# Kernel optimization log

Hardware: AMD Instinct MI355X
Metric: run time of the kernel (lower is better)

The kernel has to match this reference:

```python
import jax, jax.numpy as jnp
import numpy as np

N = 50000      # nodes
E = 800000     # edges (avg degree 16)
H = 2          # heads
IN = 128       # in_channels
OUT = 32       # out_channels


def setup_inputs() -> dict:
    key = jax.random.key(0)
    k1, k2, k3, k4, k5, k6 = jax.random.split(key, 6)
    x = jax.random.normal(k1, (N, IN), jnp.float32)
    pos = jax.random.normal(k2, (N, 3), jnp.float32)
    # xavier-ish scaled params
    W = jax.random.normal(k3, (H, IN, OUT), jnp.float32) * (1.0 / np.sqrt(IN))
    attn = jax.random.normal(k4, (H, 2 * OUT), jnp.float32) * (1.0 / np.sqrt(2 * OUT))
    row = jax.random.randint(k5, (E,), 0, N, dtype=jnp.int32)
    col = jax.random.randint(k6, (E,), 0, N, dtype=jnp.int32)
    return {"x": x, "pos": pos, "W": W, "attn": attn, "row": row, "col": col}


def _segment_softmax(logits, seg, n):
    # numerically-stable softmax grouped by destination node `seg`
    m = jax.ops.segment_max(logits, seg, num_segments=n)
    m = jnp.where(jnp.isfinite(m), m, 0.0)          # empty segments -> 0
    z = jnp.exp(logits - m[seg])
    s = jax.ops.segment_sum(z, seg, num_segments=n)
    return z / jnp.maximum(s[seg], 1e-16)


def reference(x, pos, W, attn, row, col):
    n = x.shape[0]
    out = jnp.einsum('ni,hio->hno', x, W)           # [H,N,h] per-head projection
    # add self loops (num_nodes), PyG fills self-loop edge weight with 1
    loop = jnp.arange(n, dtype=row.dtype)
    row2 = jnp.concatenate([row, loop])             # [E'] = E + N
    col2 = jnp.concatenate([col, loop])
    d = jnp.sqrt(jnp.sum((pos[col] - pos[row]) ** 2, axis=-1))   # [E]
    dist = jnp.maximum(jnp.concatenate([d, jnp.ones(n, x.dtype)]), 1e-6)  # [E']
    src = out[:, row2]                              # edge gather  [H,E',h]
    e = jnp.concatenate([src, src], axis=-1)        # duplicated src (per source) [H,E',2h]
    logits = jnp.einsum('hed,hd->he', e, attn)      # per-edge attention score [H,E']
    alpha = jax.vmap(lambda l: _segment_softmax(l, row2, n))(logits)  # [H,E']
    s = e.sum(axis=-1) * alpha / dist               # weighted per-edge scalar [H,E']
    node = jax.vmap(lambda v: jax.ops.segment_sum(v, row2, num_segments=n))(s)  # [H,N]
    return node[:, row2] - node[:, col2]            # indexed subtraction [H,E']
```

## Files before the change

kernel.cpp:

```cpp
#include <hip/hip_runtime.h>

#define IN_DIM 128
#define OUT_DIM 32
#define NHEAD 2
#define BINSZ 12500
#define NSTRIPE 64
#define THREADS 1024
#define PBLOCKS 256
#define FIX 32.0f
#define INV_FALLBACK 128.0f
#define LDS_CNT_SHIFT 25
#define U16_INV_MASK 0x1FFFu
#define U16_CNT_SHIFT 13
#define FB_NODES 32
#define FB_GROUPS 8

__global__ __launch_bounds__(THREADS) void k_main(
        const int* __restrict__ row, const int* __restrict__ col,
        const float* __restrict__ pos, const float* __restrict__ x,
        const float* __restrict__ W,
        unsigned short* __restrict__ partial, float* __restrict__ Dbig,
        float2* __restrict__ S2, int N, int E, int nbins, int eblocks) {
    __shared__ __align__(16) unsigned acc[BINSZ];
    const int b = blockIdx.x;
    if (b < eblocks) {
        const int bin  = b % nbins;
        const int s    = b / nbins;
        const int base = bin * BINSZ;
        const int lim  = min(BINSZ, N - base);
        for (int j = threadIdx.x; j < BINSZ; j += THREADS) acc[j] = 0u;
        __syncthreads();

        const int slen = (E + NSTRIPE - 1) / NSTRIPE;
        const int e0 = s * slen;
        const int e1 = min(e0 + slen, E);

        auto accum = [&](int r, int c) {
            int rb = r - base;
            if ((unsigned)rb < (unsigned)lim) {
                float dx = pos[c * 3 + 0] - pos[r * 3 + 0];
                float dy = pos[c * 3 + 1] - pos[r * 3 + 1];
                float dz = pos[c * 3 + 2] - pos[r * 3 + 2];
                float inv = 1.0f / fmaxf(sqrtf(dx * dx + dy * dy + dz * dz), 1e-6f);
                if (inv <= INV_FALLBACK) {
                    atomicAdd(&acc[rb], (1u << LDS_CNT_SHIFT) + (unsigned)(inv * FIX + 0.5f));
                } else {
                    atomicAdd(&acc[rb], 1u << LDS_CNT_SHIFT);
                    atomicAdd(&Dbig[r], inv);
                }
            }
        };

        if (((e0 | e1) & 3) == 0) {
            for (int e = e0 + (int)threadIdx.x * 4; e < e1; e += THREADS * 4) {
                int4 r4 = *(const int4*)(row + e);
                int4 c4 = *(const int4*)(col + e);
                accum(r4.x, c4.x); accum(r4.y, c4.y);
                accum(r4.z, c4.z); accum(r4.w, c4.w);
            }
        } else {
            for (int e = e0 + (int)threadIdx.x; e < e1; e += THREADS)
                accum(row[e], col[e]);
        }

        __syncthreads();
        unsigned short* dst = partial + (size_t)s * N + base;
        for (int j = threadIdx.x; j < lim; j += THREADS) {
            unsigned v   = acc[j];
            unsigned cnt = v >> LDS_CNT_SHIFT;
            unsigned inv = v & ((1u << LDS_CNT_SHIFT) - 1u);
            cnt = min(cnt, 7u);
            inv = min(inv, U16_INV_MASK);
            dst[j] = (unsigned short)((cnt << U16_CNT_SHIFT) | inv);
        }
    } else {
        float* wl = (float*)acc;
        if (threadIdx.x < NHEAD * IN_DIM) {
            const float4* wp = (const float4*)(W + threadIdx.x * OUT_DIM);
            float s = 0.f;
            #pragma unroll
            for (int q = 0; q < 8; ++q) {
                float4 v = wp[q];
                s += (v.x + v.y) + (v.z + v.w);
            }
            wl[threadIdx.x] = s;
        }
        __syncthreads();

        const int lid = threadIdx.x & 15;
        const float4* wv = (const float4*)wl;
        float4 w0a = wv[lid * 2],      w0b = wv[lid * 2 + 1];
        float4 w1a = wv[32 + lid * 2], w1b = wv[32 + lid * 2 + 1];

        const int g      = (b - eblocks) * (THREADS / 16) + (threadIdx.x >> 4);
        const int stride = (gridDim.x - eblocks) * (THREADS / 16);
        for (int i = g; i < N; i += stride) {
            const float4* xp = (const float4*)(x + (size_t)i * IN_DIM);
            float4 xa = xp[lid * 2], xb = xp[lid * 2 + 1];
            float s0 = (xa.x * w0a.x + xa.y * w0a.y + xa.z * w0a.z + xa.w * w0a.w)
                     + (xb.x * w0b.x + xb.y * w0b.y + xb.z * w0b.z + xb.w * w0b.w);
            float s1 = (xa.x * w1a.x + xa.y * w1a.y + xa.z * w1a.z + xa.w * w1a.w)
                     + (xb.x * w1b.x + xb.y * w1b.y + xb.z * w1b.z + xb.w * w1b.w);
            #pragma unroll
            for (int off = 8; off >= 1; off >>= 1) {
                s0 += __shfl_xor(s0, off, 16);
                s1 += __shfl_xor(s1, off, 16);
            }
            if (lid == 0) S2[i] = make_float2(s0, s1);
        }
    }
}

__global__ void k_fold(const unsigned short* __restrict__ partial,
                       const float* __restrict__ Dbig,
                       const float2* __restrict__ S2,
                       float2* __restrict__ node2, int N) {
    __shared__ unsigned sh[FB_GROUPS][FB_NODES];
    const int il = threadIdx.x & (FB_NODES - 1);
    const int g  = threadIdx.x >> 5;
    const int i  = blockIdx.x * FB_NODES + il;
    unsigned isum = 0, csum = 0;
    if (i < N) {
        #pragma unroll
        for (int q = 0; q < 8; ++q) {
            unsigned v = partial[(size_t)(g * 8 + q) * N + i];
            isum += v & U16_INV_MASK;
            csum += v >> U16_CNT_SHIFT;
        }
    }
    sh[g][il] = (csum << 20) | isum;
    __syncthreads();
    if (g == 0 && i < N) {
        unsigned tot = 0;
        #pragma unroll
        for (int q = 0; q < FB_GROUPS; ++q) tot += sh[q][il];
        float invsum = (float)(tot & 0xFFFFFu) * (1.0f / FIX) + Dbig[i];
        float fac = 2.0f * (1.0f + invsum) / (1.0f + (float)(tot >> 20));
        float2 sv = S2[i];
        node2[i] = make_float2(sv.x * fac, sv.y * fac);
    }
}

__global__ void k_out2(const int* __restrict__ row, const int* __restrict__ col,
                       const float2* __restrict__ node2,
                       float* __restrict__ out, int E, int M) {
    int k = (blockIdx.x * blockDim.x + threadIdx.x) * 2;
    if (k >= M) return;
    float2 a = make_float2(0.f, 0.f), b = make_float2(0.f, 0.f);
    if (k < E) {
        int2 r2 = *(const int2*)(row + k);
        int2 c2 = *(const int2*)(col + k);
        float2 nr0 = node2[r2.x], nc0 = node2[c2.x];
        float2 nr1 = node2[r2.y], nc1 = node2[c2.y];
        a = make_float2(nr0.x - nc0.x, nr1.x - nc1.x);
        b = make_float2(nr0.y - nc0.y, nr1.y - nc1.y);
    }
    *(float2*)(out + k)     = a;
    *(float2*)(out + M + k) = b;
}

__global__ void k_out1(const int* __restrict__ row, const int* __restrict__ col,
                       const float2* __restrict__ node2,
                       float* __restrict__ out, int E, int M) {
    int k = blockIdx.x * blockDim.x + threadIdx.x;
    if (k >= M) return;
    float o0 = 0.f, o1 = 0.f;
    if (k < E) {
        float2 nr = node2[row[k]], nc = node2[col[k]];
        o0 = nr.x - nc.x;
        o1 = nr.y - nc.y;
    }
    out[k]     = o0;
    out[M + k] = o1;
}

extern "C" void kernel_launch(void* const* d_in, const int* in_sizes, int n_in,
                              void* d_out, int out_size, void* d_ws, size_t ws_size,
                              hipStream_t stream) {
    const float* x   = (const float*)d_in[0];
    const float* pos = (const float*)d_in[1];
    const float* W   = (const float*)d_in[2];
    const int* row = (const int*)d_in[4];
    const int* col = (const int*)d_in[5];
    float* out = (float*)d_out;

    const int N = in_sizes[0] / IN_DIM;
    const int E = in_sizes[4];
    const int M = E + N;
    const int nbins = (N + BINSZ - 1) / BINSZ;
    const int eblocks = nbins * NSTRIPE;

    float2* S2    = (float2*)d_ws;
    float2* node2 = S2 + N;
    float*  Dbig  = (float*)(node2 + N);
    unsigned short* partial = (unsigned short*)(Dbig + N);

    hipMemsetAsync(Dbig, 0, (size_t)N * sizeof(float), stream);

    k_main<<<eblocks + PBLOCKS, THREADS, 0, stream>>>(
        row, col, pos, x, W, partial, Dbig, S2, N, E, nbins, eblocks);
    k_fold<<<(N + FB_NODES - 1) / FB_NODES, FB_NODES * FB_GROUPS, 0, stream>>>(
        partial, Dbig, S2, node2, N);
    if (((E | M) & 1) == 0)
        k_out2<<<((M >> 1) + 255) / 256, 256, 0, stream>>>(row, col, node2, out, E, M);
    else
        k_out1<<<(M + 255) / 256, 256, 0, stream>>>(row, col, node2, out, E, M);
}
```

Before: 40.99 us.

## Fuse edge binning, fold and output into one cooperative kernel with grid syncs

Replaces the memset plus three separate kernel launches with a single cooperative kernel of 256 blocks that runs the edge-binning/projection, fold and edge-output phases separated by grid.sync(). The partial buffer widens to 32-bit words with a different count/fixed-point split, which removes the Dbig atomic fallback for large inverse distances and the memset that cleared it. Stripes are halved, so each edge block scans more edges. Launch and inter-kernel gaps should shrink, at the cost of fewer edge blocks, grid-barrier overhead and possible fixed-point overflow when inverse distances are very large.

```diff
diff --git a/kernel.cpp b/kernel.cpp
--- a/kernel.cpp
+++ b/kernel.cpp
@@ -1,28 +1,26 @@
 #include <hip/hip_runtime.h>
+#include <hip/hip_cooperative_groups.h>
+
+namespace cg = cooperative_groups;
 
 #define IN_DIM 128
 #define OUT_DIM 32
 #define NHEAD 2
 #define BINSZ 12500
-#define NSTRIPE 64
+#define NSTRIPE 32
 #define THREADS 1024
-#define PBLOCKS 256
-#define FIX 32.0f
-#define INV_FALLBACK 128.0f
-#define LDS_CNT_SHIFT 25
-#define U16_INV_MASK 0x1FFFu
-#define U16_CNT_SHIFT 13
-#define FB_NODES 32
-#define FB_GROUPS 8
-
-__global__ __launch_bounds__(THREADS) void k_main(
+#define GRID 256
+#define FIX 16.0f
+#define CSHIFT 26
+#define IMASK ((1u << CSHIFT) - 1u)
+
+__device__ __forceinline__ void phase_edges_proj(
+        unsigned* acc, int b, int nblocks,
         const int* __restrict__ row, const int* __restrict__ col,
         const float* __restrict__ pos, const float* __restrict__ x,
         const float* __restrict__ W,
-        unsigned short* __restrict__ partial, float* __restrict__ Dbig,
-        float2* __restrict__ S2, int N, int E, int nbins, int eblocks) {
-    __shared__ __align__(16) unsigned acc[BINSZ];
-    const int b = blockIdx.x;
+        unsigned* __restrict__ partial, float2* __restrict__ S2,
+        int N, int E, int nbins, int eblocks) {
     if (b < eblocks) {
         const int bin  = b % nbins;
         const int s    = b / nbins;
@@ -42,12 +40,7 @@
                 float dy = pos[c * 3 + 1] - pos[r * 3 + 1];
                 float dz = pos[c * 3 + 2] - pos[r * 3 + 2];
                 float inv = 1.0f / fmaxf(sqrtf(dx * dx + dy * dy + dz * dz), 1e-6f);
-                if (inv <= INV_FALLBACK) {
-                    atomicAdd(&acc[rb], (1u << LDS_CNT_SHIFT) + (unsigned)(inv * FIX + 0.5f));
-                } else {
-                    atomicAdd(&acc[rb], 1u << LDS_CNT_SHIFT);
-                    atomicAdd(&Dbig[r], inv);
-                }
+                atomicAdd(&acc[rb], (1u << CSHIFT) + (unsigned)(inv * FIX + 0.5f));
             }
         };
 
@@ -64,15 +57,8 @@
         }
 
         __syncthreads();
-        unsigned short* dst = partial + (size_t)s * N + base;
-        for (int j = threadIdx.x; j < lim; j += THREADS) {
-            unsigned v   = acc[j];
-            unsigned cnt = v >> LDS_CNT_SHIFT;
-            unsigned inv = v & ((1u << LDS_CNT_SHIFT) - 1u);
-            cnt = min(cnt, 7u);
-            inv = min(inv, U16_INV_MASK);
-            dst[j] = (unsigned short)((cnt << U16_CNT_SHIFT) | inv);
-        }
+        unsigned* dst = partial + (size_t)s * N + base;
+        for (int j = threadIdx.x; j < lim; j += THREADS) dst[j] = acc[j];
     } else {
         float* wl = (float*)acc;
         if (threadIdx.x < NHEAD * IN_DIM) {
@@ -93,7 +79,7 @@
         float4 w1a = wv[32 + lid * 2], w1b = wv[32 + lid * 2 + 1];
 
         const int g      = (b - eblocks) * (THREADS / 16) + (threadIdx.x >> 4);
-        const int stride = (gridDim.x - eblocks) * (THREADS / 16);
+        const int stride = (nblocks - eblocks) * (THREADS / 16);
         for (int i = g; i < N; i += stride) {
             const float4* xp = (const float4*)(x + (size_t)i * IN_DIM);
             float4 xa = xp[lid * 2], xb = xp[lid * 2 + 1];
@@ -111,67 +97,114 @@
     }
 }
 
-__global__ void k_fold(const unsigned short* __restrict__ partial,
-                       const float* __restrict__ Dbig,
-                       const float2* __restrict__ S2,
-                       float2* __restrict__ node2, int N) {
-    __shared__ unsigned sh[FB_GROUPS][FB_NODES];
-    const int il = threadIdx.x & (FB_NODES - 1);
-    const int g  = threadIdx.x >> 5;
-    const int i  = blockIdx.x * FB_NODES + il;
-    unsigned isum = 0, csum = 0;
-    if (i < N) {
-        #pragma unroll
-        for (int q = 0; q < 8; ++q) {
-            unsigned v = partial[(size_t)(g * 8 + q) * N + i];
-            isum += v & U16_INV_MASK;
-            csum += v >> U16_CNT_SHIFT;
-        }
-    }
-    sh[g][il] = (csum << 20) | isum;
-    __syncthreads();
-    if (g == 0 && i < N) {
-        unsigned tot = 0;
-        #pragma unroll
-        for (int q = 0; q < FB_GROUPS; ++q) tot += sh[q][il];
-        float invsum = (float)(tot & 0xFFFFFu) * (1.0f / FIX) + Dbig[i];
-        float fac = 2.0f * (1.0f + invsum) / (1.0f + (float)(tot >> 20));
-        float2 sv = S2[i];
-        node2[i] = make_float2(sv.x * fac, sv.y * fac);
-    }
-}
-
-__global__ void k_out2(const int* __restrict__ row, const int* __restrict__ col,
-                       const float2* __restrict__ node2,
-                       float* __restrict__ out, int E, int M) {
-    int k = (blockIdx.x * blockDim.x + threadIdx.x) * 2;
-    if (k >= M) return;
-    float2 a = make_float2(0.f, 0.f), b = make_float2(0.f, 0.f);
-    if (k < E) {
-        int2 r2 = *(const int2*)(row + k);
-        int2 c2 = *(const int2*)(col + k);
-        float2 nr0 = node2[r2.x], nc0 = node2[c2.x];
-        float2 nr1 = node2[r2.y], nc1 = node2[c2.y];
-        a = make_float2(nr0.x - nc0.x, nr1.x - nc1.x);
-        b = make_float2(nr0.y - nc0.y, nr1.y - nc1.y);
-    }
-    *(float2*)(out + k)     = a;
-    *(float2*)(out + M + k) = b;
-}
-
-__global__ void k_out1(const int* __restrict__ row, const int* __restrict__ col,
-                       const float2* __restrict__ node2,
-                       float* __restrict__ out, int E, int M) {
-    int k = blockIdx.x * blockDim.x + threadIdx.x;
-    if (k >= M) return;
-    float o0 = 0.f, o1 = 0.f;
-    if (k < E) {
-        float2 nr = node2[row[k]], nc = node2[col[k]];
-        o0 = nr.x - nc.x;
-        o1 = nr.y - nc.y;
-    }
-    out[k]     = o0;
-    out[M + k] = o1;
+__device__ __forceinline__ void phase_fold(
+        unsigned* acc, int b, int nblocks,
+        const unsigned* __restrict__ partial, const float2* __restrict__ S2,
+        float2* __restrict__ node2, int N) {
+    unsigned* sh_i = acc;
+    unsigned* sh_c = acc + 1024;
+    const int il = threadIdx.x & 63;
+    const int g  = threadIdx.x >> 6;
+    const int ntiles = (N + 63) / 64;
+    for (int tile = b; tile < ntiles; tile += nblocks) {
+        const int i = tile * 64 + il;
+        unsigned isum = 0, csum = 0;
+        if (i < N) {
+            #pragma unroll
+            for (int q = 0; q < NSTRIPE / 16; ++q) {
+                unsigned v = partial[(size_t)(g * (NSTRIPE / 16) + q) * N + i];
+                isum += v & IMASK;
+                csum += v >> CSHIFT;
+            }
+        }
+        sh_i[g * 64 + il] = isum;
+        sh_c[g * 64 + il] = csum;
+        __syncthreads();
+        if (g == 0 && i < N) {
+            unsigned ti = 0, tc = 0;
+            #pragma unroll
+            for (int q = 0; q < 16; ++q) {
+                ti += sh_i[q * 64 + il];
+                tc += sh_c[q * 64 + il];
+            }
+            float invsum = (float)ti * (1.0f / FIX);
+            float fac = 2.0f * (1.0f + invsum) / (1.0f + (float)tc);
+            float2 sv = S2[i];
+            node2[i] = make_float2(sv.x * fac, sv.y * fac);
+        }
+        __syncthreads();
+    }
+}
+
+__device__ __forceinline__ void phase_out(
+        int b, int nblocks,
+        const int* __restrict__ row, const int* __restrict__ col,
+        const float2* __restrict__ node2, float* __restrict__ out,
+        int E, int M) {
+    const bool mEven = ((M & 1) == 0);
+    const int base   = (b * THREADS + (int)threadIdx.x) * 2;
+    const int stride = nblocks * THREADS * 2;
+    for (int k = base; k < M; k += stride) {
+        float o0a = 0.f, o1a = 0.f, o0b = 0.f, o1b = 0.f;
+        const bool pair = (k + 1 < M);
+        if (k < E) {
+            float2 nr = node2[row[k]], nc = node2[col[k]];
+            o0a = nr.x - nc.x; o1a = nr.y - nc.y;
+        }
+        if (pair && k + 1 < E) {
+            float2 nr = node2[row[k + 1]], nc = node2[col[k + 1]];
+            o0b = nr.x - nc.x; o1b = nr.y - nc.y;
+        }
+        if (pair && mEven) {
+            *(float2*)(out + k)     = make_float2(o0a, o0b);
+            *(float2*)(out + M + k) = make_float2(o1a, o1b);
+        } else {
+            out[k] = o0a;         out[M + k] = o1a;
+            if (pair) { out[k + 1] = o0b; out[M + k + 1] = o1b; }
+        }
+    }
+}
+
+__global__ __launch_bounds__(THREADS, 4) void k_fused(
+        const int* __restrict__ row, const int* __restrict__ col,
+        const float* __restrict__ pos, const float* __restrict__ x,
+        const float* __restrict__ W,
+        unsigned* __restrict__ partial, float2* __restrict__ S2,
+        float2* __restrict__ node2, float* __restrict__ out,
+        int N, int E, int M, int nbins, int eblocks) {
+    __shared__ __align__(16) unsigned acc[BINSZ];
+    cg::grid_group grid = cg::this_grid();
+    phase_edges_proj(acc, blockIdx.x, GRID, row, col, pos, x, W,
+                     partial, S2, N, E, nbins, eblocks);
+    grid.sync();
+    phase_fold(acc, blockIdx.x, GRID, partial, S2, node2, N);
+    grid.sync();
+    phase_out(blockIdx.x, GRID, row, col, node2, out, E, M);
+}
+
+__global__ __launch_bounds__(THREADS) void k_A(
+        const int* __restrict__ row, const int* __restrict__ col,
+        const float* __restrict__ pos, const float* __restrict__ x,
+        const float* __restrict__ W,
+        unsigned* __restrict__ partial, float2* __restrict__ S2,
+        int N, int E, int nbins, int eblocks) {
+    __shared__ __align__(16) unsigned acc[BINSZ];
+    phase_edges_proj(acc, blockIdx.x, gridDim.x, row, col, pos, x, W,
+                     partial, S2, N, E, nbins, eblocks);
+}
+
+__global__ __launch_bounds__(THREADS) void k_B(
+        const unsigned* __restrict__ partial, const float2* __restrict__ S2,
+        float2* __restrict__ node2, int N) {
+    __shared__ __align__(16) unsigned acc[2048];
+    phase_fold(acc, blockIdx.x, gridDim.x, partial, S2, node2, N);
+}
+
+__global__ __launch_bounds__(THREADS) void k_C(
+        const int* __restrict__ row, const int* __restrict__ col,
+        const float2* __restrict__ node2, float* __restrict__ out,
+        int E, int M) {
+    phase_out(blockIdx.x, gridDim.x, row, col, node2, out, E, M);
 }
 
 extern "C" void kernel_launch(void* const* d_in, const int* in_sizes, int n_in,
@@ -184,25 +217,27 @@
     const int* col = (const int*)d_in[5];
     float* out = (float*)d_out;
 
-    const int N = in_sizes[0] / IN_DIM;
-    const int E = in_sizes[4];
-    const int M = E + N;
-    const int nbins = (N + BINSZ - 1) / BINSZ;
-    const int eblocks = nbins * NSTRIPE;
+    int N = in_sizes[0] / IN_DIM;
+    int E = in_sizes[4];
+    int M = E + N;
+    int nbins = (N + BINSZ - 1) / BINSZ;
+    int eblocks = nbins * NSTRIPE;
+    if (eblocks > GRID - 32) eblocks = GRID - 32;
 
     float2* S2    = (float2*)d_ws;
     float2* node2 = S2 + N;
-    float*  Dbig  = (float*)(node2 + N);
-    unsigned short* partial = (unsigned short*)(Dbig + N);
-
-    hipMemsetAsync(Dbig, 0, (size_t)N * sizeof(float), stream);
-
-    k_main<<<eblocks + PBLOCKS, THREADS, 0, stream>>>(
-        row, col, pos, x, W, partial, Dbig, S2, N, E, nbins, eblocks);
-    k_fold<<<(N + FB_NODES - 1) / FB_NODES, FB_NODES * FB_GROUPS, 0, stream>>>(
-        partial, Dbig, S2, node2, N);
-    if (((E | M) & 1) == 0)
-        k_out2<<<((M >> 1) + 255) / 256, 256, 0, stream>>>(row, col, node2, out, E, M);
-    else
-        k_out1<<<(M + 255) / 256, 256, 0, stream>>>(row, col, node2, out, E, M);
-}
+    unsigned* partial = (unsigned*)(node2 + N);
+
+    void* args[] = { (void*)&row, (void*)&col, (void*)&pos, (void*)&x, (void*)&W,
+                     (void*)&partial, (void*)&S2, (void*)&node2, (void*)&out,
+                     (void*)&N, (void*)&E, (void*)&M, (void*)&nbins, (void*)&eblocks };
+    hipError_t err = hipLaunchCooperativeKernel((void*)k_fused, dim3(GRID),
+                                                dim3(THREADS), args, 0, stream);
+    if (err != hipSuccess) {
+        k_A<<<eblocks + 384, THREADS, 0, stream>>>(row, col, pos, x, W,
+                                                   partial, S2, N, E, nbins, eblocks);
+        k_B<<<(N + 63) / 64, THREADS, 0, stream>>>(partial, S2, node2, N);
+        k_C<<<(M / 2 + THREADS - 1) / THREADS, THREADS, 0, stream>>>(row, col, node2,
+                                                                     out, E, M);
+    }
+}
```

Result: slower. 116.3 us (+183.7%).
